# Optimization experiments

Hardware: AMD Instinct MI355X
Metric: run time of the kernel (lower is better)

The kernel has to match this reference:

```python
import jax, jax.numpy as jnp
import numpy as np

BS, N, DX, DE, STEPS = 32, 64, 8, 5, 50


def setup_inputs() -> dict:
    key = jax.random.key(0)
    kx, ke, km, kg, kwx, kwe = jax.random.split(key, 6)
    # one-hot node states [bs, n, dx]
    x_lab = jax.random.randint(kx, (BS, N), 0, DX)
    X = jax.nn.one_hot(x_lab, DX, dtype=jnp.float32)
    # symmetric one-hot edge states [bs, n, n, de], zero diagonal
    e_lab = jax.random.randint(ke, (BS, N, N), 0, DE)
    e_lab = jnp.triu(e_lab, 1)
    e_lab = e_lab + jnp.swapaxes(e_lab, 1, 2)
    E = jax.nn.one_hot(e_lab, DE, dtype=jnp.float32)
    # variable-size graphs: first `length` nodes valid
    lengths = jax.random.randint(km, (BS,), N // 2, N + 1)
    node_mask = jnp.arange(N)[None, :] < lengths[:, None]
    gammas = jax.random.uniform(kg, (STEPS,), minval=1e-3, maxval=2e-2)
    # stub denoising network weights (stand-in for the graph transformer `net`)
    Wx = jax.random.normal(kwx, (DX, DX)) * 0.5
    We = jax.random.normal(kwe, (DE, DE)) * 0.5
    return {"X": X, "E": E, "node_mask": node_mask, "gammas": gammas, "Wx": Wx, "We": We}


def _langevin(X, E, gammas, Wx, We, node_mask):
    bs, n, dx = X.shape
    de = E.shape[-1]
    nm = node_mask.astype(X.dtype)                    # [bs, n]
    em = nm[:, :, None] * nm[:, None, :]              # [bs, n, n]
    em = em * (1.0 - jnp.eye(n, dtype=X.dtype))       # zero diagonal
    iu = jnp.triu(jnp.ones((n, n), dtype=bool), 1)    # strict upper triangle
    key0 = jax.random.key(42)

    def step(carry, inp):
        Xc, Ec = carry
        gamma, k = inp
        kx, ke = jax.random.split(jax.random.fold_in(key0, k))
        # --- stub `net` forward: per-class linear map + softmax ---
        predX = jax.nn.softmax(Xc @ Wx, axis=-1) * gamma          # pred.X * gamma
        predE = jax.nn.softmax(Ec @ We, axis=-1) * gamma          # pred.E * gamma
        predE = 0.5 * (predE + jnp.swapaxes(predE, 1, 2))         # symmetric edges
        # --- scatter_(argmax, 0); scatter_(argmax, clamp(1-sum,0)); normalize ---
        ohx = jax.nn.one_hot(jnp.argmax(Xc, -1), dx, dtype=Xc.dtype)
        ohe = jax.nn.one_hot(jnp.argmax(Ec, -1), de, dtype=Ec.dtype)
        predX = predX * (1.0 - ohx)
        predE = predE * (1.0 - ohe)
        predX = predX + ohx * jnp.maximum(1.0 - predX.sum(-1, keepdims=True), 0.0)
        predE = predE + ohe * jnp.maximum(1.0 - predE.sum(-1, keepdims=True), 0.0)
        predX = predX / predX.sum(-1, keepdims=True)
        predE = predE / predE.sum(-1, keepdims=True)
        # --- categorical sample (Gumbel-argmax), one-hot, symmetrize, mask ---
        sx = jnp.argmax(jnp.log(predX) + jax.random.gumbel(kx, predX.shape), -1)
        se = jnp.argmax(jnp.log(predE) + jax.random.gumbel(ke, predE.shape), -1)
        se = jnp.where(iu[None], se, 0)
        se = se + jnp.swapaxes(se, 1, 2)
        Xn = jax.nn.one_hot(sx, dx, dtype=Xc.dtype) * nm[:, :, None]
        En = jax.nn.one_hot(se, de, dtype=Ec.dtype) * em[..., None]
        return (Xn, En), (Xc, Ec, Xn, En)

    ks = jnp.arange(STEPS)
    _, (outX, outE, totX, totE) = jax.lax.scan(step, (X, E), (gammas, ks))
    tr = lambda a: jnp.moveaxis(a, 0, 1)             # [steps,bs,...] -> [bs,steps,...]
    return tr(totX), tr(totE), tr(outX), tr(outE)


def reference(X, E, node_mask, gammas, Wx, We):
    return _langevin(X, E, gammas, Wx, We, node_mask)
```

## Files before the change

### kernel.cpp

```cpp
#include <hip/hip_runtime.h>
#include <stdint.h>

#pragma clang fp contract(off)

#define STEPS 50
#define BSZ 32
#define NN 64
#define DXC 8
#define DEC 5
#define OFF_TOTE 819200UL
#define OFF_OUTX 33587200UL
#define OFF_OUTE 34406400UL

#define NPAIR 2016
#define EDGE_CHAINS 64512
#define WS_KEYS 0UL
#define WS_CL   1024UL
#define WS_CB   130048UL
#define WS_GE   388096UL
#define WS_GN   64900096UL
#define WS_S2E  68176896UL
#define WS_S2N  71402496UL
#define WS_NEED 71504896UL

__device__ __forceinline__ uint32_t rotl32(uint32_t x, int d) {
  return (x << d) | (x >> (32 - d));
}

__device__ __forceinline__ void tf2x32(uint32_t k0, uint32_t k1,
                                       uint32_t x0, uint32_t x1,
                                       uint32_t& o0, uint32_t& o1) {
  uint32_t ks2 = k0 ^ k1 ^ 0x1BD11BDAu;
  x0 += k0; x1 += k1;
#define TF_R(r) { x0 += x1; x1 = rotl32(x1, (r)); x1 ^= x0; }
  TF_R(13) TF_R(15) TF_R(26) TF_R(6)
  x0 += k1; x1 += ks2 + 1u;
  TF_R(17) TF_R(29) TF_R(16) TF_R(24)
  x0 += ks2; x1 += k0 + 2u;
  TF_R(13) TF_R(15) TF_R(26) TF_R(6)
  x0 += k0; x1 += k1 + 3u;
  TF_R(17) TF_R(29) TF_R(16) TF_R(24)
  x0 += k1; x1 += ks2 + 4u;
  TF_R(13) TF_R(15) TF_R(26) TF_R(6)
  x0 += ks2; x1 += k0 + 5u;
#undef TF_R
  o0 = x0; o1 = x1;
}

__device__ __forceinline__ float logf_cr(float x) { return (float)log((double)x); }
__device__ __forceinline__ float expf_cr(float x) { return (float)exp((double)x); }

__device__ __forceinline__ float gumbel_inl(uint32_t k0, uint32_t k1,
                                            uint32_t idx) {
  uint32_t o0, o1;
  tf2x32(k0, k1, 0u, idx, o0, o1);
  uint32_t bits = o0 ^ o1;
  float uf = __uint_as_float((bits >> 9) | 0x3f800000u) - 1.0f;
  float u = fmaxf(uf, 1.1754943508222875e-38f);
  return -logf_cr(-logf_cr(u));
}
__device__ __attribute__((noinline)) float gumbel_part(uint32_t k0, uint32_t k1,
                                                       uint32_t idx) {
  return gumbel_inl(k0, k1, idx);
}

__device__ __forceinline__ bool detect_bf16(const void* X) {
  const uint16_t* u = (const uint16_t*)X;
  int c = 0;
  for (int i = 0; i < 16; ++i) c += (u[i] == 0x3F80u);
  return c >= 2;
}

__device__ __forceinline__ float ld(const void* p, size_t i, bool bf) {
  if (bf) return __uint_as_float(((uint32_t)((const uint16_t*)p)[i]) << 16);
  return ((const float*)p)[i];
}
__device__ __forceinline__ void st(void* p, size_t i, bool bf, float v) {
  if (bf) ((uint16_t*)p)[i] = (uint16_t)(__float_as_uint(v) >> 16);
  else ((float*)p)[i] = v;
}
__device__ __forceinline__ void stv4(void* p, size_t e4, bool bf,
                                     float a, float b, float c, float d) {
  if (!bf) {
    float4 v; v.x = a; v.y = b; v.z = c; v.w = d;
    ((float4*)p)[e4] = v;
  } else {
    ushort4 v;
    v.x = (uint16_t)(__float_as_uint(a) >> 16);
    v.y = (uint16_t)(__float_as_uint(b) >> 16);
    v.z = (uint16_t)(__float_as_uint(c) >> 16);
    v.w = (uint16_t)(__float_as_uint(d) >> 16);
    ((ushort4*)p)[e4] = v;
  }
}
__device__ __forceinline__ void cpy4(void* dst, const void* src, size_t de4,
                                     size_t se4, bool bf) {
  if (!bf) ((float4*)dst)[de4] = ((const float4*)src)[se4];
  else ((uint2*)dst)[de4] = ((const uint2*)src)[se4];
}

__device__ __forceinline__ bool read_mask(const void* mp, int idx) {
  const uint8_t* m8 = (const uint8_t*)mp;
  uint8_t b1 = m8[1];
  if (b1 == 0) return ((const uint32_t*)mp)[idx] != 0;
  if (b1 == 0x3F) return ((const uint16_t*)mp)[idx] != 0;
  return m8[idx] != 0;
}

template <int D>
__device__ void fill_logp(const void* __restrict__ W, bool bf, float gamma,
                          int c, float* __restrict__ out) {
  float t[D];
  for (int d = 0; d < D; ++d) t[d] = ld(W, c * D + d, bf);
  float m = t[0];
  for (int d = 1; d < D; ++d) m = fmaxf(m, t[d]);
  float u[D];
  for (int d = 0; d < D; ++d) u[d] = expf_cr(t[d] - m);
  float s = 0.0f;
  for (int d = 0; d < D; ++d) s += u[d];
  float p[D];
  for (int d = 0; d < D; ++d) p[d] = (u[d] / s) * gamma;
  p[c] = 0.0f;
  float s1 = 0.0f;
  for (int d = 0; d < D; ++d) s1 += p[d];
  float r = fmaxf(1.0f - s1, 0.0f);
  p[c] = r;
  float s2 = 0.0f;
  for (int d = 0; d < D; ++d) s2 += p[d];
  for (int d = 0; d < D; ++d) out[d] = logf_cr(p[d] / s2);
}

__device__ __forceinline__ void pair_decode(int q, int& lo, int& hi) {
  lo = 0; int rem = q;
  while (rem >= 63 - lo) { rem -= 63 - lo; lo++; }
  hi = lo + 1 + rem;
}

__global__ void key_kernel(uint8_t* __restrict__ ws) {
  int t = threadIdx.x;
  uint32_t* wk = (uint32_t*)(ws + WS_KEYS);
  if (t == 0) wk[200] = 0u;
  if (t < STEPS) {
    uint32_t f0, f1, a0, a1;
    tf2x32(0u, 42u, 0u, (uint32_t)t, f0, f1);
    tf2x32(f0, f1, 0u, 0u, a0, a1);
    wk[2 * t] = a0; wk[2 * t + 1] = a1;
    tf2x32(f0, f1, 0u, 1u, a0, a1);
    wk[100 + 2 * t] = a0; wk[101 + 2 * t] = a1;
  }
}

__global__ __launch_bounds__(256) void compact_kernel(const void* __restrict__ M,
                                                      uint8_t* __restrict__ ws) {
  int chain = blockIdx.x * 256 + threadIdx.x;
  if (chain >= EDGE_CHAINS) return;
  int b = chain / NPAIR, q = chain % NPAIR, lo, hi;
  pair_decode(q, lo, hi);
  if (read_mask(M, b * NN + lo) && read_mask(M, b * NN + hi)) {
    uint32_t slot = atomicAdd((uint32_t*)(ws + WS_KEYS) + 200, 1u);
    ((uint16_t*)(ws + WS_CL))[slot] = (uint16_t)chain;
    ((uint32_t*)(ws + WS_CB))[slot] =
        (uint32_t)(((b * NN + lo) * NN + hi) * DEC);
  }
}

__global__ __launch_bounds__(256) void gumbel_kernel(const void* __restrict__ M,
                                                     uint8_t* __restrict__ ws) {
  const uint32_t* keys = (const uint32_t*)(ws + WS_KEYS);
  const int tid = threadIdx.x;
  if (blockIdx.y < 250) {
    uint32_t cnt = keys[200];
    uint32_t slot = blockIdx.x * 256 + tid;
    if (slot >= cnt) return;
    int slab = blockIdx.y, k = slab / DEC, d = slab - k * DEC;
    uint32_t ctr = ((const uint32_t*)(ws + WS_CB))[slot] + (uint32_t)d;
    ((float*)(ws + WS_GE))[(size_t)slab * EDGE_CHAINS + slot] =
        gumbel_inl(keys[100 + 2 * k], keys[101 + 2 * k], ctr);
  } else {
    int idx = ((int)blockIdx.y - 250) * 252 + (int)blockIdx.x;
    if (idx >= 3200) return;
    int slab = idx >> 3;
    int node = ((idx & 7) << 8) + tid;
    if (!read_mask(M, node)) return;
    int k = slab >> 3, d = slab & 7;
    ((float*)(ws + WS_GN))[(size_t)slab * 2048 + node] =
        gumbel_inl(keys[2 * k], keys[2 * k + 1], (uint32_t)(node * DXC + d));
  }
}

__global__ __launch_bounds__(256) void chain_kernel(
    const void* __restrict__ X, const void* __restrict__ E,
    const void* __restrict__ M, const void* __restrict__ gammas,
    const void* __restrict__ Wx, const void* __restrict__ We,
    uint8_t* __restrict__ ws) {
  __shared__ float stab[STEPS * DXC * DXC];
  const bool edge_blk = blockIdx.x < 252;
  const int t = threadIdx.x;
  const bool bf = detect_bf16(X);

  if (edge_blk) {
    for (int task = t; task < STEPS * DEC; task += 256)
      fill_logp<DEC>(We, bf, ld(gammas, task / DEC, bf), task % DEC,
                     &stab[task * DEC]);
  } else {
    for (int task = t; task < STEPS * DXC; task += 256)
      fill_logp<DXC>(Wx, bf, ld(gammas, task / DXC, bf), task % DXC,
                     &stab[task * DXC]);
  }
  __syncthreads();

  if (edge_blk) {
    uint32_t cnt = ((const uint32_t*)(ws + WS_KEYS))[200];
    uint32_t slot = blockIdx.x * 256 + t;
    if (slot >= cnt) return;
    int chain = (int)((const uint16_t*)(ws + WS_CL))[slot];
    int b = chain / NPAIR, q = chain - b * NPAIR;
    uint32_t crow = ((const uint32_t*)(ws + WS_CB))[slot];
    int cur = 0;
    float bst = ld(E, crow, bf);
    for (int d = 1; d < DEC; ++d) {
      float v = ld(E, (size_t)crow + d, bf);
      if (v > bst) { bst = v; cur = d; }
    }
    const float* ge = (const float*)(ws + WS_GE);
    uint8_t* s2e = ws + WS_S2E;
    for (int k = 0; k < STEPS; ++k) {
      const float* le = stab + (k * DEC + cur) * DEC;
      float bs = -3.0e38f; int nxt = 0;
      for (int d = 0; d < DEC; ++d) {
        float s = le[d] + ge[(size_t)(k * DEC + d) * EDGE_CHAINS + slot];
        if (s > bs) { bs = s; nxt = d; }
      }
      s2e[(size_t)(b * STEPS + k) * NPAIR + q] = (uint8_t)nxt;
      cur = nxt;
    }
  } else {
    int node = (int)(blockIdx.x - 252) * 256 + t;
    if (!read_mask(M, node)) return;
    int b = node >> 6, i = node & 63;
    int cur = 0;
    float bst = ld(X, (size_t)node * DXC, bf);
    for (int d = 1; d < DXC; ++d) {
      float v = ld(X, (size_t)node * DXC + d, bf);
      if (v > bst) { bst = v; cur = d; }
    }
    const float* gn = (const float*)(ws + WS_GN);
    uint8_t* s2n = ws + WS_S2N;
    for (int k = 0; k < STEPS; ++k) {
      const float* le = stab + (k * DXC + cur) * DXC;
      float bs = -3.0e38f; int nxt = 0;
      for (int d = 0; d < DXC; ++d) {
        float s = le[d] + gn[(size_t)(k * DXC + d) * 2048 + node];
        if (s > bs) { bs = s; nxt = d; }
      }
      s2n[(size_t)(b * STEPS + k) * 64 + i] = (uint8_t)nxt;
      cur = nxt;
    }
  }
}

__global__ __launch_bounds__(256) void write_kernel(
    const void* __restrict__ X, const void* __restrict__ E,
    const void* __restrict__ M, const uint8_t* __restrict__ ws,
    void* __restrict__ out) {
  __shared__ uint8_t cur_g[4096];
  __shared__ uint8_t pre_g[4096];
  __shared__ uint8_t sc[NPAIR];
  __shared__ uint8_t sp_[NPAIR];
  __shared__ uint8_t sn[3200];
  __shared__ uint8_t vf[64];
  const bool bf = detect_bf16(X);
  const int t = threadIdx.x;

  if (blockIdx.x < 1600) {
    int slab = blockIdx.x;
    int b = slab / STEPS, k = slab % STEPS;
    if (t < 64) vf[t] = read_mask(M, b * NN + t) ? 1 : 0;
    const uint8_t* s2e = ws + WS_S2E;
    for (int x = t; x < 504; x += 256) {
      ((uint32_t*)sc)[x] = ((const uint32_t*)(s2e + (size_t)slab * NPAIR))[x];
      if (k > 0)
        ((uint32_t*)sp_)[x] =
            ((const uint32_t*)(s2e + (size_t)(slab - 1) * NPAIR))[x];
    }
    __syncthreads();
    for (int ij = t; ij < 4096; ij += 256) {
      int i = ij >> 6, j = ij & 63;
      uint8_t c = 0xFF, p = 0xFF;
      if (i != j && vf[i] && vf[j]) {
        int lo = i < j ? i : j, hi = i < j ? j : i;
        int q = 63 * lo - ((lo * (lo - 1)) >> 1) + hi - lo - 1;
        c = sc[q];
        if (k > 0) p = sp_[q];
      }
      cur_g[ij] = c; pre_g[ij] = p;
    }
    __syncthreads();
    size_t base = (size_t)slab * 20480;
    for (int f = t; f < 5120; f += 256) {
      int e0 = f * 4;
      float v[4];
#pragma unroll
      for (int m = 0; m < 4; ++m) {
        int e = e0 + m, ij = e / 5, d = e - ij * 5;
        v[m] = (d == (int)cur_g[ij]) ? 1.0f : 0.0f;
      }
      stv4(out, (OFF_TOTE + base) / 4 + f, bf, v[0], v[1], v[2], v[3]);
    }
    if (k == 0) {
      size_t src4 = (size_t)b * 5120;
      for (int f = t; f < 5120; f += 256)
        cpy4(out, E, (OFF_OUTE + base) / 4 + f, src4 + f, bf);
    } else {
      for (int f = t; f < 5120; f += 256) {
        int e0 = f * 4;
        float v[4];
#pragma unroll
        for (int m = 0; m < 4; ++m) {
          int e = e0 + m, ij = e / 5, d = e - ij * 5;
          v[m] = (d == (int)pre_g[ij]) ? 1.0f : 0.0f;
        }
        stv4(out, (OFF_OUTE + base) / 4 + f, bf, v[0], v[1], v[2], v[3]);
      }
    }
  } else {
    int b = (int)blockIdx.x - 1600;
    if (t < 64) vf[t] = read_mask(M, b * NN + t) ? 1 : 0;
    for (int x = t; x < 800; x += 256)
      ((uint32_t*)sn)[x] =
          ((const uint32_t*)(ws + WS_S2N + (size_t)b * STEPS * 64))[x];
    __syncthreads();
    size_t base0 = (size_t)b * 25600;
    for (int f = t; f < 6400; f += 256) {
      int e0 = f * 4;
      int k = e0 >> 9, i = (e0 >> 3) & 63;
      int s = (int)sn[k * 64 + i];
      bool va = vf[i] != 0;
      float v[4];
#pragma unroll
      for (int m = 0; m < 4; ++m) {
        int d = (e0 + m) & 7;
        v[m] = (va && d == s) ? 1.0f : 0.0f;
      }
      stv4(out, base0 / 4 + f, bf, v[0], v[1], v[2], v[3]);
    }
    for (int f = t; f < 6400; f += 256) {
      int e0 = f * 4;
      int k = e0 >> 9, i = (e0 >> 3) & 63;
      if (k == 0) {
        cpy4(out, X, (OFF_OUTX + base0) / 4 + f,
             ((size_t)b * 512 + (size_t)(e0 & 511)) / 4, bf);
      } else {
        int s = (int)sn[(k - 1) * 64 + i];
        bool va = vf[i] != 0;
        float v[4];
#pragma unroll
        for (int m = 0; m < 4; ++m) {
          int d = (e0 + m) & 7;
          v[m] = (va && d == s) ? 1.0f : 0.0f;
        }
        stv4(out, (OFF_OUTX + base0) / 4 + f, bf, v[0], v[1], v[2], v[3]);
      }
    }
  }
}

__global__ __launch_bounds__(256) void lang_kernel(
    const void* __restrict__ X, const void* __restrict__ E,
    const void* __restrict__ M, const void* __restrict__ gammas,
    const void* __restrict__ Wx, const void* __restrict__ We,
    void* __restrict__ out) {
  __shared__ uint32_t skeys[STEPS * 2];
  __shared__ float stab[STEPS * DXC * DXC];
  const bool edge_blk = blockIdx.x < 512;
  const int t = threadIdx.x;
  const bool bf = detect_bf16(X);

  if (t < STEPS) {
    uint32_t f0, f1, a0, a1;
    tf2x32(0u, 42u, 0u, (uint32_t)t, f0, f1);
    tf2x32(f0, f1, 0u, edge_blk ? 1u : 0u, a0, a1);
    skeys[2 * t] = a0; skeys[2 * t + 1] = a1;
  }
  if (edge_blk) {
    for (int task = t; task < STEPS * DEC; task += 256) {
      int k = task / DEC, c = task % DEC;
      fill_logp<DEC>(We, bf, ld(gammas, k, bf), c, &stab[(k * DEC + c) * DEC]);
    }
  } else {
    for (int task = t; task < STEPS * DXC; task += 256) {
      int k = task / DXC, c = task % DXC;
      fill_logp<DXC>(Wx, bf, ld(gammas, k, bf), c, &stab[(k * DXC + c) * DXC]);
    }
  }
  __syncthreads();

  if (edge_blk) {
    int tid = blockIdx.x * 256 + threadIdx.x;
    int b = tid >> 12, rem = tid & 4095, i = rem >> 6, j = rem & 63;
    bool valid = (i != j) && read_mask(M, b * NN + i) && read_mask(M, b * NN + j);
    int lo = i < j ? i : j, hi = i < j ? j : i;
    int cur = 0;
    if (valid) {
      size_t crow = (((size_t)(b * NN + lo)) * NN + hi) * DEC;
      float bst = ld(E, crow, bf);
      for (int d = 1; d < DEC; ++d) {
        float v = ld(E, crow + d, bf);
        if (v > bst) { bst = v; cur = d; }
      }
    }
    uint32_t base = (uint32_t)((((b * NN) + lo) * NN + hi) * DEC);
#pragma clang loop unroll(disable)
    for (int k = 0; k < STEPS; ++k) {
      size_t tp = ((((size_t)b * STEPS + k) * NN + i) * NN + j) * DEC;
      if (k == 0) {
        for (int d = 0; d < DEC; ++d)
          st(out, OFF_OUTE + tp + d, bf, ld(E, (size_t)tid * DEC + d, bf));
      } else {
        for (int d = 0; d < DEC; ++d)
          st(out, OFF_OUTE + tp + d, bf, (valid && d == cur) ? 1.0f : 0.0f);
      }
      int nxt = 0;
      if (valid) {
        const float* le = stab + (k * DEC + cur) * DEC;
        uint32_t k0 = skeys[2 * k], k1 = skeys[2 * k + 1];
        float bst = -3.0e38f;
        for (int d = 0; d < DEC; ++d) {
          float s = le[d] + gumbel_part(k0, k1, base + (uint32_t)d);
          if (s > bst) { bst = s; nxt = d; }
        }
      }
      for (int d = 0; d < DEC; ++d)
        st(out, OFF_TOTE + tp + d, bf, (valid && d == nxt) ? 1.0f : 0.0f);
      cur = nxt;
    }
  } else {
    int tid = (int)(blockIdx.x - 512) * 256 + threadIdx.x;
    if (tid >= BSZ * NN) return;
    int b = tid >> 6, i = tid & 63;
    bool valid = read_mask(M, tid);
    int cur = 0;
    {
      float bst = ld(X, (size_t)tid * DXC, bf);
      for (int d = 1; d < DXC; ++d) {
        float v = ld(X, (size_t)tid * DXC + d, bf);
        if (v > bst) { bst = v; cur = d; }
      }
    }
    uint32_t base = (uint32_t)(tid * DXC);
#pragma clang loop unroll(disable)
    for (int k = 0; k < STEPS; ++k) {
      size_t tp = (((size_t)b * STEPS + k) * NN + i) * DXC;
      if (k == 0) {
        for (int d = 0; d < DXC; ++d)
          st(out, OFF_OUTX + tp + d, bf, ld(X, (size_t)tid * DXC + d, bf));
      } else {
        for (int d = 0; d < DXC; ++d)
          st(out, OFF_OUTX + tp + d, bf, (valid && d == cur) ? 1.0f : 0.0f);
      }
      int nxt = 0;
      if (valid) {
        const float* lx = stab + (k * DXC + cur) * DXC;
        uint32_t k0 = skeys[2 * k], k1 = skeys[2 * k + 1];
        float bst = -3.0e38f;
        for (int d = 0; d < DXC; ++d) {
          float s = lx[d] + gumbel_part(k0, k1, base + (uint32_t)d);
          if (s > bst) { bst = s; nxt = d; }
        }
      }
      for (int d = 0; d < DXC; ++d)
        st(out, tp + d, bf, (valid && d == nxt) ? 1.0f : 0.0f);
      cur = nxt;
    }
  }
}

extern "C" void kernel_launch(void* const* d_in, const int* in_sizes, int n_in,
                              void* d_out, int out_size, void* d_ws, size_t ws_size,
                              hipStream_t stream) {
  (void)out_size;
  const void* X = d_in[0];
  const void* E = d_in[1];
  const void* M = d_in[2];
  const void* G = d_in[3];
  const void* Wx = d_in[4];
  const void* We = d_in[5];
  for (int i = 0; i < n_in && i < 6; ++i) {
    switch (in_sizes[i]) {
      case 16384:  X = d_in[i]; break;
      case 655360: E = d_in[i]; break;
      case 2048:   M = d_in[i]; break;
      case 50:     G = d_in[i]; break;
      case 64:     Wx = d_in[i]; break;
      case 25:     We = d_in[i]; break;
      default: break;
    }
  }
  if (ws_size >= WS_NEED) {
    uint8_t* ws = (uint8_t*)d_ws;
    hipLaunchKernelGGL(key_kernel, dim3(1), dim3(64), 0, stream, ws);
    hipLaunchKernelGGL(compact_kernel, dim3(252), dim3(256), 0, stream, M, ws);
    hipLaunchKernelGGL(gumbel_kernel, dim3(252, 263), dim3(256), 0, stream,
                       M, ws);
    hipLaunchKernelGGL(chain_kernel, dim3(260), dim3(256), 0, stream,
                       X, E, M, G, Wx, We, ws);
    hipLaunchKernelGGL(write_kernel, dim3(1632), dim3(256), 0, stream,
                       X, E, M, ws, d_out);
  } else {
    hipLaunchKernelGGL(lang_kernel, dim3(520), dim3(256), 0, stream,
                       X, E, M, G, Wx, We, d_out);
  }
}
```

Measured before the change: 433.2 us.

## Fuse Gumbel generation into chain kernel with per-class lanes and shuffles

Drops the separate Gumbel-precompute kernel, which wrote about 64 MB of noise to workspace, and instead generates each Gumbel value inside the sampling chain. Each chain is spread across 5 (edge) or 8 (node) lanes, and the argmax is reduced with wave shuffles. The log-probability tables and RNG keys are now computed once in a prep kernel and staged into shared memory. This removes heavy global-memory write and read traffic and raises parallelism, but puts the Threefry hashing on the serial 50-step dependency chain.

```diff
diff --git a/kernel.cpp b/kernel.cpp
--- a/kernel.cpp
+++ b/kernel.cpp
@@ -14,14 +14,15 @@
 
 #define NPAIR 2016
 #define EDGE_CHAINS 64512
+#define EDGE_BLOCKS 1344
 #define WS_KEYS 0UL
-#define WS_CL   1024UL
-#define WS_CB   130048UL
-#define WS_GE   388096UL
-#define WS_GN   64900096UL
-#define WS_S2E  68176896UL
-#define WS_S2N  71402496UL
-#define WS_NEED 71504896UL
+#define WS_STE  1024UL
+#define WS_STN  6144UL
+#define WS_CL   18944UL
+#define WS_CB   147968UL
+#define WS_S2E  406016UL
+#define WS_S2N  3631616UL
+#define WS_NEED 3734016UL
 
 __device__ __forceinline__ uint32_t rotl32(uint32_t x, int d) {
   return (x << d) | (x >> (32 - d));
@@ -136,8 +137,12 @@
   hi = lo + 1 + rem;
 }
 
-__global__ void key_kernel(uint8_t* __restrict__ ws) {
-  int t = threadIdx.x;
+__global__ __launch_bounds__(256) void prep_kernel(
+    const void* __restrict__ X, const void* __restrict__ gammas,
+    const void* __restrict__ Wx, const void* __restrict__ We,
+    uint8_t* __restrict__ ws) {
+  const int t = threadIdx.x;
+  const bool bf = detect_bf16(X);
   uint32_t* wk = (uint32_t*)(ws + WS_KEYS);
   if (t == 0) wk[200] = 0u;
   if (t < STEPS) {
@@ -148,6 +153,12 @@
     tf2x32(f0, f1, 0u, 1u, a0, a1);
     wk[100 + 2 * t] = a0; wk[101 + 2 * t] = a1;
   }
+  for (int task = t; task < STEPS * DEC; task += 256)
+    fill_logp<DEC>(We, bf, ld(gammas, task / DEC, bf), task % DEC,
+                   (float*)(ws + WS_STE) + task * DEC);
+  for (int task = t; task < STEPS * DXC; task += 256)
+    fill_logp<DXC>(Wx, bf, ld(gammas, task / DXC, bf), task % DXC,
+                   (float*)(ws + WS_STN) + task * DXC);
 }
 
 __global__ __launch_bounds__(256) void compact_kernel(const void* __restrict__ M,
@@ -164,96 +175,93 @@
   }
 }
 
-__global__ __launch_bounds__(256) void gumbel_kernel(const void* __restrict__ M,
-                                                     uint8_t* __restrict__ ws) {
-  const uint32_t* keys = (const uint32_t*)(ws + WS_KEYS);
-  const int tid = threadIdx.x;
-  if (blockIdx.y < 250) {
-    uint32_t cnt = keys[200];
-    uint32_t slot = blockIdx.x * 256 + tid;
-    if (slot >= cnt) return;
-    int slab = blockIdx.y, k = slab / DEC, d = slab - k * DEC;
-    uint32_t ctr = ((const uint32_t*)(ws + WS_CB))[slot] + (uint32_t)d;
-    ((float*)(ws + WS_GE))[(size_t)slab * EDGE_CHAINS + slot] =
-        gumbel_inl(keys[100 + 2 * k], keys[101 + 2 * k], ctr);
-  } else {
-    int idx = ((int)blockIdx.y - 250) * 252 + (int)blockIdx.x;
-    if (idx >= 3200) return;
-    int slab = idx >> 3;
-    int node = ((idx & 7) << 8) + tid;
-    if (!read_mask(M, node)) return;
-    int k = slab >> 3, d = slab & 7;
-    ((float*)(ws + WS_GN))[(size_t)slab * 2048 + node] =
-        gumbel_inl(keys[2 * k], keys[2 * k + 1], (uint32_t)(node * DXC + d));
-  }
-}
-
 __global__ __launch_bounds__(256) void chain_kernel(
     const void* __restrict__ X, const void* __restrict__ E,
-    const void* __restrict__ M, const void* __restrict__ gammas,
-    const void* __restrict__ Wx, const void* __restrict__ We,
-    uint8_t* __restrict__ ws) {
+    const void* __restrict__ M, uint8_t* __restrict__ ws) {
   __shared__ float stab[STEPS * DXC * DXC];
-  const bool edge_blk = blockIdx.x < 252;
+  __shared__ uint32_t skeys[STEPS * 2];
+  const bool edge_blk = blockIdx.x < EDGE_BLOCKS;
   const int t = threadIdx.x;
   const bool bf = detect_bf16(X);
+  const uint32_t* wk = (const uint32_t*)(ws + WS_KEYS);
 
   if (edge_blk) {
-    for (int task = t; task < STEPS * DEC; task += 256)
-      fill_logp<DEC>(We, bf, ld(gammas, task / DEC, bf), task % DEC,
-                     &stab[task * DEC]);
-  } else {
-    for (int task = t; task < STEPS * DXC; task += 256)
-      fill_logp<DXC>(Wx, bf, ld(gammas, task / DXC, bf), task % DXC,
-                     &stab[task * DXC]);
+    for (int x = t; x < STEPS * DEC * DEC; x += 256)
+      stab[x] = ((const float*)(ws + WS_STE))[x];
+    if (t < STEPS * 2) skeys[t] = wk[100 + t];
+  } else {
+    for (int x = t; x < STEPS * DXC * DXC; x += 256)
+      stab[x] = ((const float*)(ws + WS_STN))[x];
+    if (t < STEPS * 2) skeys[t] = wk[t];
   }
   __syncthreads();
 
+  const int lane = t & 63;
   if (edge_blk) {
-    uint32_t cnt = ((const uint32_t*)(ws + WS_KEYS))[200];
-    uint32_t slot = blockIdx.x * 256 + t;
+    if (lane >= 60) return;
+    const uint32_t cnt = wk[200];
+    int grp = lane / 5, d = lane - grp * 5, gb = (t & ~63) % 64 + grp * 5;
+    gb = grp * 5;
+    uint32_t slot = (uint32_t)((blockIdx.x * 4 + (t >> 6)) * 12 + grp);
     if (slot >= cnt) return;
     int chain = (int)((const uint16_t*)(ws + WS_CL))[slot];
+    uint32_t cb = ((const uint32_t*)(ws + WS_CB))[slot];
     int b = chain / NPAIR, q = chain - b * NPAIR;
-    uint32_t crow = ((const uint32_t*)(ws + WS_CB))[slot];
+    float v = ld(E, (size_t)cb + d, bf);
     int cur = 0;
-    float bst = ld(E, crow, bf);
-    for (int d = 1; d < DEC; ++d) {
-      float v = ld(E, (size_t)crow + d, bf);
-      if (v > bst) { bst = v; cur = d; }
-    }
-    const float* ge = (const float*)(ws + WS_GE);
+    {
+      float bst = __shfl(v, gb, 64);
+      for (int j = 1; j < DEC; ++j) {
+        float vj = __shfl(v, gb + j, 64);
+        if (vj > bst) { bst = vj; cur = j; }
+      }
+    }
     uint8_t* s2e = ws + WS_S2E;
+#pragma clang loop unroll(disable)
     for (int k = 0; k < STEPS; ++k) {
-      const float* le = stab + (k * DEC + cur) * DEC;
-      float bs = -3.0e38f; int nxt = 0;
-      for (int d = 0; d < DEC; ++d) {
-        float s = le[d] + ge[(size_t)(k * DEC + d) * EDGE_CHAINS + slot];
-        if (s > bs) { bs = s; nxt = d; }
-      }
-      s2e[(size_t)(b * STEPS + k) * NPAIR + q] = (uint8_t)nxt;
+      float g = gumbel_part(skeys[2 * k], skeys[2 * k + 1], cb + (uint32_t)d);
+      float s = stab[(k * DEC + cur) * DEC + d] + g;
+      int nxt = 0;
+      {
+        float bst = __shfl(s, gb, 64);
+        for (int j = 1; j < DEC; ++j) {
+          float sj = __shfl(s, gb + j, 64);
+          if (sj > bst) { bst = sj; nxt = j; }
+        }
+      }
+      if (d == 0) s2e[(size_t)(b * STEPS + k) * NPAIR + q] = (uint8_t)nxt;
       cur = nxt;
     }
   } else {
-    int node = (int)(blockIdx.x - 252) * 256 + t;
+    int grp = lane >> 3, d = lane & 7, gb = grp * 8;
+    int node = ((int)blockIdx.x - EDGE_BLOCKS) * 32 + (t >> 3);
+    if (node >= BSZ * NN) return;
     if (!read_mask(M, node)) return;
     int b = node >> 6, i = node & 63;
+    float v = ld(X, (size_t)node * DXC + d, bf);
     int cur = 0;
-    float bst = ld(X, (size_t)node * DXC, bf);
-    for (int d = 1; d < DXC; ++d) {
-      float v = ld(X, (size_t)node * DXC + d, bf);
-      if (v > bst) { bst = v; cur = d; }
-    }
-    const float* gn = (const float*)(ws + WS_GN);
+    {
+      float bst = __shfl(v, gb, 64);
+      for (int j = 1; j < DXC; ++j) {
+        float vj = __shfl(v, gb + j, 64);
+        if (vj > bst) { bst = vj; cur = j; }
+      }
+    }
     uint8_t* s2n = ws + WS_S2N;
+#pragma clang loop unroll(disable)
     for (int k = 0; k < STEPS; ++k) {
-      const float* le = stab + (k * DXC + cur) * DXC;
-      float bs = -3.0e38f; int nxt = 0;
-      for (int d = 0; d < DXC; ++d) {
-        float s = le[d] + gn[(size_t)(k * DXC + d) * 2048 + node];
-        if (s > bs) { bs = s; nxt = d; }
-      }
-      s2n[(size_t)(b * STEPS + k) * 64 + i] = (uint8_t)nxt;
+      float g = gumbel_part(skeys[2 * k], skeys[2 * k + 1],
+                            (uint32_t)(node * DXC + d));
+      float s = stab[(k * DXC + cur) * DXC + d] + g;
+      int nxt = 0;
+      {
+        float bst = __shfl(s, gb, 64);
+        for (int j = 1; j < DXC; ++j) {
+          float sj = __shfl(s, gb + j, 64);
+          if (sj > bst) { bst = sj; nxt = j; }
+        }
+      }
+      if (d == 0) s2n[(size_t)(b * STEPS + k) * 64 + i] = (uint8_t)nxt;
       cur = nxt;
     }
   }
@@ -498,12 +506,11 @@
   }
   if (ws_size >= WS_NEED) {
     uint8_t* ws = (uint8_t*)d_ws;
-    hipLaunchKernelGGL(key_kernel, dim3(1), dim3(64), 0, stream, ws);
+    hipLaunchKernelGGL(prep_kernel, dim3(1), dim3(256), 0, stream,
+                       X, G, Wx, We, ws);
     hipLaunchKernelGGL(compact_kernel, dim3(252), dim3(256), 0, stream, M, ws);
-    hipLaunchKernelGGL(gumbel_kernel, dim3(252, 263), dim3(256), 0, stream,
-                       M, ws);
-    hipLaunchKernelGGL(chain_kernel, dim3(260), dim3(256), 0, stream,
-                       X, E, M, G, Wx, We, ws);
+    hipLaunchKernelGGL(chain_kernel, dim3(EDGE_BLOCKS + 64), dim3(256), 0,
+                       stream, X, E, M, ws);
     hipLaunchKernelGGL(write_kernel, dim3(1632), dim3(256), 0, stream,
                        X, E, M, ws, d_out);
   } else {
```

New measurement: 436.6 us. About the same (+0.8%).
